# Kernel tuning notes

Hardware: AMD Instinct MI355X
Metric: run time of the kernel (lower is better)

Reference implementation:

```python
import jax, jax.numpy as jnp
import numpy as np

N, E, D, H = 100000, 1250000, 64, 128
EPS = 1e-5


def sage_bn_relu(x, src, dst, W_self, b_self, W_neigh, gamma, beta):
    # mean aggregation over in-neighbors (DGL SAGEConv 'mean')
    n = x.shape[0]
    deg = jax.ops.segment_sum(jnp.ones((src.shape[0],), x.dtype), dst, num_segments=n)
    agg = jax.ops.segment_sum(x[src], dst, num_segments=n)  # [N, d]
    neigh = agg / jnp.maximum(deg, 1.0)[:, None]             # zero in-degree -> 0
    h = x @ W_self + b_self + neigh @ W_neigh                # fc_self + fc_neigh
    # BatchNorm1d (training-mode batch statistics, biased variance)
    mu = h.mean(0)
    var = jnp.mean((h - mu) ** 2, axis=0)
    h = (h - mu) * jax.lax.rsqrt(var + EPS) * gamma + beta
    return jax.nn.relu(h)  # dropout omitted (deterministic eval)


def setup_inputs() -> dict:
    key = jax.random.key(0)
    ks = jax.random.split(key, 32)
    inp = {
        "x": jax.random.normal(ks[0], (N, D), jnp.float32),
        "src": jax.random.randint(ks[1], (E,), 0, N),
        "dst": jax.random.randint(ks[2], (E,), 0, N),
    }
    dims = [(D, H), (H, H), (H, H)]
    k = 3
    for i, (din, dout) in enumerate(dims):
        s = 1.0 / np.sqrt(din)
        inp[f"W_self{i}"] = jax.random.uniform(ks[k], (din, dout), jnp.float32, -s, s); k += 1
        inp[f"b_self{i}"] = jnp.zeros((dout,), jnp.float32)
        inp[f"W_neigh{i}"] = jax.random.uniform(ks[k], (din, dout), jnp.float32, -s, s); k += 1
        inp[f"gamma{i}"] = jnp.ones((dout,), jnp.float32)
        inp[f"beta{i}"] = jnp.zeros((dout,), jnp.float32)
    s = 1.0 / np.sqrt(H)
    inp["Wc"] = jax.random.uniform(ks[k], (H, 2), jnp.float32, -s, s)
    inp["bc"] = jnp.zeros((2,), jnp.float32)
    return inp


def reference(x, src, dst,
              W_self0, b_self0, W_neigh0, gamma0, beta0,
              W_self1, b_self1, W_neigh1, gamma1, beta1,
              W_self2, b_self2, W_neigh2, gamma2, beta2,
              Wc, bc):
    h = sage_bn_relu(x, src, dst, W_self0, b_self0, W_neigh0, gamma0, beta0)
    h = sage_bn_relu(h, src, dst, W_self1, b_self1, W_neigh1, gamma1, beta1)
    h = sage_bn_relu(h, src, dst, W_self2, b_self2, W_neigh2, gamma2, beta2)
    return h @ Wc + bc  # [N, 2]
```

## Files before the change

kernel.cpp:

```cpp
#include <hip/hip_runtime.h>


#define N_NODES 100000
#define N_EDGES 1250000
#define NB 1563
#define BSZ 64
#define CAP 1024
#define BPART 256
#define INVN (1.0f / 100000.0f)

typedef short bf16x8 __attribute__((ext_vector_type(8)));
typedef float f32x4 __attribute__((ext_vector_type(4)));
typedef unsigned short u16x8 __attribute__((ext_vector_type(8)));
typedef unsigned short u16x4 __attribute__((ext_vector_type(4)));

__device__ __forceinline__ float bf2f(unsigned short u) {
  union { unsigned int i; float f; } c; c.i = ((unsigned int)u) << 16; return c.f;
}
__device__ __forceinline__ unsigned short f2bf(float f) {
  union { float f; unsigned int i; } c; c.f = f;
  unsigned int r = (c.i + 0x7FFFu + ((c.i >> 16) & 1u)) >> 16;
  return (unsigned short)r;
}
__device__ __forceinline__ void bn_st(const float* stats, const float* gam,
                                      const float* bet, int c, float& s, float& t) {
  float sum = stats[c] + stats[256 + c] + stats[512 + c] + stats[768 + c];
  float sq  = stats[128 + c] + stats[384 + c] + stats[640 + c] + stats[896 + c];
  float mu = sum * INVN;
  float var = sq * INVN - mu * mu;
  s = gam[c] * rsqrtf(var + 1e-5f);
  t = bet[c] - mu * s;
}
__device__ __forceinline__ void gload_lds16(const void* g, void* l) {
  __builtin_amdgcn_global_load_lds(
      (const __attribute__((address_space(1))) unsigned int*)g,
      (__attribute__((address_space(3))) unsigned int*)l, 16, 0, 0);
}

__global__ __launch_bounds__(256) void k_prep(
    const float* __restrict__ x, unsigned short* __restrict__ x16,
    const float* __restrict__ W0s, const float* __restrict__ W0n,
    const float* __restrict__ W1s, const float* __restrict__ W1n,
    const float* __restrict__ W2s, const float* __restrict__ W2n,
    unsigned short* __restrict__ wt, float* __restrict__ stats3,
    const int* __restrict__ dst, int* __restrict__ hist, int E) {
  __shared__ int hh[NB];
  int blk = blockIdx.x, t = threadIdx.x;
  if (blk < 6250) {
    int i = blk * 256 + t;
    float4 v = ((const float4*)x)[i];
    u16x4 o;
    o.x = f2bf(v.x); o.y = f2bf(v.y); o.z = f2bf(v.z); o.w = f2bf(v.w);
    ((u16x4*)x16)[i] = o;
  } else if (blk < 6570) {
    int i = (blk - 6250) * 256 + t;
    if (i < 16384) {
      const float* W = (i < 8192) ? W0s : W0n;
      unsigned short* o = wt + (i < 8192 ? 0 : 8192);
      int j = i & 8191;
      int c = j >> 6, k = j & 63;
      o[j] = f2bf(W[k * 128 + c]);
    } else {
      int j = i - 16384;
      int sel = j >> 14;
      j &= 16383;
      const float* W = (sel == 0) ? W1s : (sel == 1) ? W1n : (sel == 2) ? W2s : W2n;
      unsigned short* o = wt + 16384 + sel * 16384;
      int c = j >> 7, k = j & 127;
      o[j] = f2bf(W[k * 128 + c]);
    }
  } else if (blk == 6570) {
    for (int i = t; i < 3 * 1024; i += 256) stats3[i] = 0.f;
  } else {
    int hb = blk - 6571;
    int chunk = (E + BPART - 1) / BPART;
    int start = hb * chunk;
    int end = min(E, start + chunk);
    for (int b = t; b < NB; b += 256) hh[b] = 0;
    __syncthreads();
    for (int e = start + t; e < end; e += 256) atomicAdd(&hh[dst[e] >> 6], 1);
    __syncthreads();
    for (int b = t; b < NB; b += 256) hist[hb * NB + b] = hh[b];
  }
}

__global__ __launch_bounds__(256) void k_scan(const int* __restrict__ hist,
                                              int* __restrict__ base,
                                              int* __restrict__ gcursor) {
  int bb = blockIdx.x * 256 + threadIdx.x;
  if (bb >= NB) return;
  int run = 0;
  for (int r0 = 0; r0 < BPART; r0 += 16) {
    int v[16];
    #pragma unroll
    for (int u = 0; u < 16; u++) v[u] = hist[(r0 + u) * NB + bb];
    #pragma unroll
    for (int u = 0; u < 16; u++) { base[(r0 + u) * NB + bb] = run; run += v[u]; }
  }
  gcursor[bb] = run;
}

__global__ __launch_bounds__(256) void k_scatter(const int* __restrict__ src,
                                                 const int* __restrict__ dst,
                                                 const int* __restrict__ base,
                                                 unsigned int* __restrict__ part, int E) {
  __shared__ int cur[NB];
  int t = threadIdx.x;
  int chunk = (E + BPART - 1) / BPART;
  int start = blockIdx.x * chunk;
  int end = min(E, start + chunk);
  for (int b = t; b < NB; b += 256) cur[b] = base[blockIdx.x * NB + b];
  __syncthreads();
  for (int e = start + t; e < end; e += 256) {
    int d = dst[e];
    int b = d >> 6;
    int pos = atomicAdd(&cur[b], 1);
    if ((unsigned)pos < (unsigned)CAP)
      part[(size_t)b * CAP + pos] = (unsigned)src[e] | ((unsigned)(d & 63) << 17);
  }
}

template <int DIN, bool BN>
__global__ __launch_bounds__(512, 8) void k_layer(
    const unsigned short* __restrict__ h, const unsigned short* __restrict__ W1t,
    const unsigned short* __restrict__ W2t, const float* __restrict__ bias,
    const unsigned int* __restrict__ part, const int* __restrict__ gcursor,
    unsigned short* __restrict__ C, float* __restrict__ stats, int M,
    const float* __restrict__ statsP, const float* __restrict__ gamP,
    const float* __restrict__ betP) {
  __shared__ unsigned short neighT[64 * DIN];
  __shared__ unsigned eord[CAP];
  __shared__ unsigned short Bs[2][128 * 32];
  __shared__ int cnt[BSZ], offv[BSZ], cur[BSZ];
  __shared__ int stealCtr;
  __shared__ float sBN[128], tBN[128];
  unsigned* eraw = (unsigned*)neighT;
  float* redS = (float*)eord;
  float* redQ = redS + 512;

  constexpr int SWZM = (DIN == 128) ? 15 : 7;
  constexpr int KS = DIN / 32;
  int t = threadIdx.x;
  int lane = t & 63, w = t >> 6;
  int l15 = lane & 15, quad = lane >> 4;
  int bkt = blockIdx.x;
  int node0 = bkt * BSZ;
  int nn = min(BSZ, M - node0);

  if (t < BSZ) cnt[t] = 0;
  if (t == 0) stealCtr = 0;
  if (BN && t < 128) bn_st(statsP, gamP, betP, t, sBN[t], tBN[t]);
  __syncthreads();

  int ec = gcursor[bkt];
  ec = max(0, min(ec, CAP));
  for (int i = t; i < ec; i += 512) {
    unsigned wd = part[(size_t)bkt * CAP + i];
    eraw[i] = wd;
    atomicAdd(&cnt[wd >> 17], 1);
  }
  __syncthreads();
  if (t < BSZ) offv[t] = cnt[t];
  __syncthreads();
  #pragma unroll
  for (int o = 1; o < BSZ; o <<= 1) {
    int xv = 0;
    if (t < BSZ && t >= o) xv = offv[t - o];
    __syncthreads();
    if (t < BSZ) offv[t] += xv;
    __syncthreads();
  }
  if (t < BSZ) { int ex = offv[t] - cnt[t]; offv[t] = ex; cur[t] = ex; }
  __syncthreads();
  for (int i = t; i < ec; i += 512) {
    unsigned wd = eraw[i];
    int p = atomicAdd(&cur[wd >> 17], 1);
    eord[p] = wd & 0x1FFFF;
  }
  __syncthreads();

  const int strip = w >> 1;
  const int ch = w & 1;
  const int row = strip * 16 + l15;
  f32x4 acc4[4];
  #pragma unroll
  for (int ct = 0; ct < 4; ct++) acc4[ct] = (f32x4){0.f, 0.f, 0.f, 0.f};
  #pragma unroll
  for (int s = 0; s < KS; s++) {
    int k0 = s * 32;
    u16x8 v = *(const u16x8*)&h[(size_t)(node0 + row) * DIN + k0 + quad * 8];
    if (BN) {
      #pragma unroll
      for (int j = 0; j < 8; j++) {
        int c = k0 + quad * 8 + j;
        v[j] = f2bf(fmaxf(fmaf(bf2f(v[j]), sBN[c], tBN[c]), 0.f));
      }
    }
    bf16x8 af = *(bf16x8*)&v;
    #pragma unroll
    for (int ct = 0; ct < 4; ct++) {
      u16x8 bv = *(const u16x8*)&W1t[(size_t)(ch * 64 + ct * 16 + l15) * DIN + k0 + quad * 8];
      acc4[ct] = __builtin_amdgcn_mfma_f32_16x16x32_bf16(af, *(bf16x8*)&bv, acc4[ct], 0, 0, 0);
    }
  }

  const int G = DIN / 8;
  int li = t & (G - 1);
  float sreg[8], treg[8];
  if (BN) {
    #pragma unroll
    for (int k = 0; k < 8; k++) { sreg[k] = sBN[li * 8 + k]; treg[k] = tBN[li * 8 + k]; }
  }
  for (;;) {
    int nd0 = 0;
    if (li == 0) nd0 = atomicAdd(&stealCtr, 1);
    int nd = __shfl(nd0, 0, G);
    if (nd >= BSZ) break;
    u16x8 o;
    if (nd >= nn) {
      #pragma unroll
      for (int k = 0; k < 8; k++) o[k] = 0;
    } else {
      int s = offv[nd], c = cnt[nd];
      int e = s + c;
      float acc[8] = {0.f, 0.f, 0.f, 0.f, 0.f, 0.f, 0.f, 0.f};
      int j = s;
      for (; j + 2 <= e; j += 2) {
        int sn0 = eord[j], sn1 = eord[j + 1];
        u16x8 v0 = *(const u16x8*)&h[(size_t)sn0 * DIN + li * 8];
        u16x8 v1 = *(const u16x8*)&h[(size_t)sn1 * DIN + li * 8];
        if (BN) {
          #pragma unroll
          for (int k = 0; k < 8; k++)
            acc[k] += fmaxf(fmaf(bf2f(v0[k]), sreg[k], treg[k]), 0.f)
                    + fmaxf(fmaf(bf2f(v1[k]), sreg[k], treg[k]), 0.f);
        } else {
          #pragma unroll
          for (int k = 0; k < 8; k++) acc[k] += bf2f(v0[k]) + bf2f(v1[k]);
        }
      }
      if (j < e) {
        int sn = eord[j];
        u16x8 v = *(const u16x8*)&h[(size_t)sn * DIN + li * 8];
        if (BN) {
          #pragma unroll
          for (int k = 0; k < 8; k++)
            acc[k] += fmaxf(fmaf(bf2f(v[k]), sreg[k], treg[k]), 0.f);
        } else {
          #pragma unroll
          for (int k = 0; k < 8; k++) acc[k] += bf2f(v[k]);
        }
      }
      float inv = 1.0f / fmaxf((float)c, 1.0f);
      #pragma unroll
      for (int k = 0; k < 8; k++) o[k] = f2bf(acc[k] * inv);
    }
    *(u16x8*)&neighT[nd * DIN + ((li * 8) ^ ((nd & SWZM) << 3))] = o;
  }

  auto stageBs = [&](int k0, int bi) {
    int r = t >> 2, c = t & 3;
    int p = c ^ ((r >> 1) & 3);
    gload_lds16(&W2t[(size_t)r * DIN + k0 + p * 8], &Bs[bi][(w * 64) * 8]);
  };
  stageBs(0, 0);
  __syncthreads();

  int cb = 0;
  #pragma unroll
  for (int s = 0; s < KS; s++) {
    if (s + 1 < KS) stageBs((s + 1) * 32, cb ^ 1);
    int cc = s * 32 + quad * 8;
    u16x8 v = *(const u16x8*)&neighT[row * DIN + (cc ^ ((row & SWZM) << 3))];
    bf16x8 af = *(bf16x8*)&v;
    #pragma unroll
    for (int ct = 0; ct < 4; ct++) {
      int brow = ch * 64 + ct * 16 + l15;
      bf16x8 bfr = *(const bf16x8*)&Bs[cb][brow * 32 + ((quad ^ ((brow >> 1) & 3)) * 8)];
      acc4[ct] = __builtin_amdgcn_mfma_f32_16x16x32_bf16(af, bfr, acc4[ct], 0, 0, 0);
    }
    if (s + 1 < KS) __syncthreads();
    cb ^= 1;
  }

  float bcol[4], ls[4], lq[4];
  #pragma unroll
  for (int ct = 0; ct < 4; ct++) {
    bcol[ct] = bias[ch * 64 + ct * 16 + l15];
    ls[ct] = 0.f; lq[ct] = 0.f;
  }
  #pragma unroll
  for (int r = 0; r < 4; r++) {
    int orow = node0 + strip * 16 + quad * 4 + r;
    if (orow < M) {
      #pragma unroll
      for (int ct = 0; ct < 4; ct++) {
        float v = acc4[ct][r] + bcol[ct];
        C[(size_t)orow * 128 + ch * 64 + ct * 16 + l15] = f2bf(v);
        ls[ct] += v; lq[ct] += v * v;
      }
    }
  }
  __syncthreads();
  #pragma unroll
  for (int ct = 0; ct < 4; ct++) {
    ls[ct] += __shfl_xor(ls[ct], 16); ls[ct] += __shfl_xor(ls[ct], 32);
    lq[ct] += __shfl_xor(lq[ct], 16); lq[ct] += __shfl_xor(lq[ct], 32);
  }
  if (quad == 0) {
    #pragma unroll
    for (int ct = 0; ct < 4; ct++) {
      redS[w * 64 + ct * 16 + l15] = ls[ct];
      redQ[w * 64 + ct * 16 + l15] = lq[ct];
    }
  }
  __syncthreads();
  if (t < 128) {
    int ch2 = t >> 6, c6 = t & 63;
    float s = 0.f, q = 0.f;
    #pragma unroll
    for (int st = 0; st < 4; st++) {
      s += redS[(st * 2 + ch2) * 64 + c6];
      q += redQ[(st * 2 + ch2) * 64 + c6];
    }
    int rep = (bkt & 3) * 256;
    atomicAdd(&stats[rep + t], s);
    atomicAdd(&stats[rep + 128 + t], q);
  }
}

__global__ void k_final(const unsigned short* __restrict__ h,
                        const float* __restrict__ statsP, const float* __restrict__ gamP,
                        const float* __restrict__ betP, const float* __restrict__ Wc,
                        const float* __restrict__ bc, float* __restrict__ out, int n) {
  int lane = threadIdx.x & 63;
  int row = blockIdx.x * (blockDim.x >> 6) + (threadIdx.x >> 6);
  if (row >= n) return;
  float acc0 = 0.f, acc1 = 0.f;
  #pragma unroll
  for (int m = 0; m < 2; m++) {
    int c = lane + 64 * m;
    float s, tt;
    bn_st(statsP, gamP, betP, c, s, tt);
    float v = bf2f(h[(size_t)row * 128 + c]);
    v = fmaxf(fmaf(v, s, tt), 0.f);
    acc0 += v * Wc[c * 2 + 0];
    acc1 += v * Wc[c * 2 + 1];
  }
  #pragma unroll
  for (int off = 32; off > 0; off >>= 1) {
    acc0 += __shfl_down(acc0, off);
    acc1 += __shfl_down(acc1, off);
  }
  if (lane == 0) {
    out[row * 2 + 0] = acc0 + bc[0];
    out[row * 2 + 1] = acc1 + bc[1];
  }
}

extern "C" void kernel_launch(void* const* d_in, const int* in_sizes, int n_in,
                              void* d_out, int out_size, void* d_ws, size_t ws_size,
                              hipStream_t stream) {
  const float* x   = (const float*)d_in[0];
  const int* src   = (const int*)d_in[1];
  const int* dst   = (const int*)d_in[2];
  const float* Wself[3] = {(const float*)d_in[3], (const float*)d_in[8],  (const float*)d_in[13]};
  const float* bself[3] = {(const float*)d_in[4], (const float*)d_in[9],  (const float*)d_in[14]};
  const float* Wngh[3]  = {(const float*)d_in[5], (const float*)d_in[10], (const float*)d_in[15]};
  const float* gam[3]   = {(const float*)d_in[6], (const float*)d_in[11], (const float*)d_in[16]};
  const float* bet[3]   = {(const float*)d_in[7], (const float*)d_in[12], (const float*)d_in[17]};
  const float* Wc = (const float*)d_in[18];
  const float* bc = (const float*)d_in[19];
  float* out = (float*)d_out;

  const int N = N_NODES, E = N_EDGES;

  unsigned short* x16 = (unsigned short*)d_ws;
  unsigned short* b0  = x16 + (size_t)N * 64;
  unsigned short* b1  = b0 + (size_t)N * 128;
  unsigned short* b2  = b1 + (size_t)N * 128;
  unsigned short* wt  = b2 + (size_t)N * 128;
  unsigned int* part  = (unsigned int*)(wt + 81920);
  int* gcursor  = (int*)(part + (size_t)NB * CAP);
  float* stats3 = (float*)(gcursor + NB);

  int* hist = (int*)b1;
  int* base = hist + (size_t)BPART * NB;

  k_prep<<<6571 + BPART, 256, 0, stream>>>(
      x, x16, Wself[0], Wngh[0], Wself[1], Wngh[1], Wself[2], Wngh[2],
      wt, stats3, dst, hist, E);

  k_scan<<<(NB + 255) / 256, 256, 0, stream>>>(hist, base, gcursor);
  k_scatter<<<BPART, 256, 0, stream>>>(src, dst, base, part, E);

  k_layer<64, false><<<NB, 512, 0, stream>>>(
      x16, wt + 0, wt + 8192, bself[0], part, gcursor, b1, stats3 + 0, N,
      nullptr, nullptr, nullptr);
  k_layer<128, true><<<NB, 512, 0, stream>>>(
      b1, wt + 16384, wt + 32768, bself[1], part, gcursor, b2, stats3 + 1024, N,
      stats3 + 0, gam[0], bet[0]);
  k_layer<128, true><<<NB, 512, 0, stream>>>(
      b2, wt + 49152, wt + 65536, bself[2], part, gcursor, b1, stats3 + 2048, N,
      stats3 + 1024, gam[1], bet[1]);

  k_final<<<(N + 3) / 4, 256, 0, stream>>>(b1, stats3 + 2048, gam[2], bet[2],
                                           Wc, bc, out, N);
}
```

Measured before the change: 410.0 us.

## Stage both weight matrices through double-buffered LDS and use wave-shuffle prefix scan

Replaces the multi-barrier LDS Hillis-Steele scan over bucket counts with a single-wave shuffle-up scan. The self-term GEMM, which loaded W1t straight from global memory before aggregation, now runs after aggregation in one 2*KS-step double-buffered loop that stages W1t and then W2t into LDS. The XOR swizzle on the B tile is dropped, which may bring LDS bank conflicts back, and one barrier before the stats reduction is removed. Keeping the self-term accumulators out of the aggregation loop may also lower register pressure.

```diff
diff --git a/kernel.cpp b/kernel.cpp
--- a/kernel.cpp
+++ b/kernel.cpp
@@ -160,17 +160,17 @@
     atomicAdd(&cnt[wd >> 17], 1);
   }
   __syncthreads();
-  if (t < BSZ) offv[t] = cnt[t];
-  __syncthreads();
-  #pragma unroll
-  for (int o = 1; o < BSZ; o <<= 1) {
-    int xv = 0;
-    if (t < BSZ && t >= o) xv = offv[t - o];
-    __syncthreads();
-    if (t < BSZ) offv[t] += xv;
-    __syncthreads();
-  }
-  if (t < BSZ) { int ex = offv[t] - cnt[t]; offv[t] = ex; cur[t] = ex; }
+  if (w == 0) {
+    int v = cnt[lane];
+    int incl = v;
+    #pragma unroll
+    for (int o = 1; o < 64; o <<= 1) {
+      int u = __shfl_up(incl, o);
+      if (lane >= o) incl += u;
+    }
+    offv[lane] = incl - v;
+    cur[lane] = incl - v;
+  }
   __syncthreads();
   for (int i = t; i < ec; i += 512) {
     unsigned wd = eraw[i];
@@ -178,31 +178,6 @@
     eord[p] = wd & 0x1FFFF;
   }
   __syncthreads();
-
-  const int strip = w >> 1;
-  const int ch = w & 1;
-  const int row = strip * 16 + l15;
-  f32x4 acc4[4];
-  #pragma unroll
-  for (int ct = 0; ct < 4; ct++) acc4[ct] = (f32x4){0.f, 0.f, 0.f, 0.f};
-  #pragma unroll
-  for (int s = 0; s < KS; s++) {
-    int k0 = s * 32;
-    u16x8 v = *(const u16x8*)&h[(size_t)(node0 + row) * DIN + k0 + quad * 8];
-    if (BN) {
-      #pragma unroll
-      for (int j = 0; j < 8; j++) {
-        int c = k0 + quad * 8 + j;
-        v[j] = f2bf(fmaxf(fmaf(bf2f(v[j]), sBN[c], tBN[c]), 0.f));
-      }
-    }
-    bf16x8 af = *(bf16x8*)&v;
-    #pragma unroll
-    for (int ct = 0; ct < 4; ct++) {
-      u16x8 bv = *(const u16x8*)&W1t[(size_t)(ch * 64 + ct * 16 + l15) * DIN + k0 + quad * 8];
-      acc4[ct] = __builtin_amdgcn_mfma_f32_16x16x32_bf16(af, *(bf16x8*)&bv, acc4[ct], 0, 0, 0);
-    }
-  }
 
   const int G = DIN / 8;
   int li = t & (G - 1);
@@ -258,28 +233,49 @@
     *(u16x8*)&neighT[nd * DIN + ((li * 8) ^ ((nd & SWZM) << 3))] = o;
   }
 
-  auto stageBs = [&](int k0, int bi) {
-    int r = t >> 2, c = t & 3;
-    int p = c ^ ((r >> 1) & 3);
-    gload_lds16(&W2t[(size_t)r * DIN + k0 + p * 8], &Bs[bi][(w * 64) * 8]);
+  const int strip = w >> 1;
+  const int ch = w & 1;
+  const int row = strip * 16 + l15;
+  f32x4 acc4[4];
+  #pragma unroll
+  for (int ct = 0; ct < 4; ct++) acc4[ct] = (f32x4){0.f, 0.f, 0.f, 0.f};
+
+  auto stageBs = [&](int s, int bi) {
+    const unsigned short* Wt = (s < KS) ? W1t : W2t;
+    int k0 = ((s < KS) ? s : s - KS) * 32;
+    int r = t >> 2, prt = t & 3;
+    gload_lds16(&Wt[(size_t)r * DIN + k0 + prt * 8], &Bs[bi][(w * 64) * 8]);
   };
   stageBs(0, 0);
   __syncthreads();
 
   int cb = 0;
   #pragma unroll
-  for (int s = 0; s < KS; s++) {
-    if (s + 1 < KS) stageBs((s + 1) * 32, cb ^ 1);
-    int cc = s * 32 + quad * 8;
-    u16x8 v = *(const u16x8*)&neighT[row * DIN + (cc ^ ((row & SWZM) << 3))];
-    bf16x8 af = *(bf16x8*)&v;
+  for (int s = 0; s < 2 * KS; s++) {
+    if (s + 1 < 2 * KS) stageBs(s + 1, cb ^ 1);
+    bf16x8 af;
+    if (s < KS) {
+      int k0 = s * 32;
+      u16x8 v = *(const u16x8*)&h[(size_t)(node0 + row) * DIN + k0 + quad * 8];
+      if (BN) {
+        #pragma unroll
+        for (int j = 0; j < 8; j++) {
+          int c = k0 + quad * 8 + j;
+          v[j] = f2bf(fmaxf(fmaf(bf2f(v[j]), sBN[c], tBN[c]), 0.f));
+        }
+      }
+      af = *(bf16x8*)&v;
+    } else {
+      int cc = (s - KS) * 32 + quad * 8;
+      u16x8 v = *(const u16x8*)&neighT[row * DIN + (cc ^ ((row & SWZM) << 3))];
+      af = *(bf16x8*)&v;
+    }
     #pragma unroll
     for (int ct = 0; ct < 4; ct++) {
-      int brow = ch * 64 + ct * 16 + l15;
-      bf16x8 bfr = *(const bf16x8*)&Bs[cb][brow * 32 + ((quad ^ ((brow >> 1) & 3)) * 8)];
+      bf16x8 bfr = *(const bf16x8*)&Bs[cb][(ch * 64 + ct * 16 + l15) * 32 + quad * 8];
       acc4[ct] = __builtin_amdgcn_mfma_f32_16x16x32_bf16(af, bfr, acc4[ct], 0, 0, 0);
     }
-    if (s + 1 < KS) __syncthreads();
+    if (s + 1 < 2 * KS) __syncthreads();
     cb ^= 1;
   }
 
@@ -301,7 +297,6 @@
       }
     }
   }
-  __syncthreads();
   #pragma unroll
   for (int ct = 0; ct < 4; ct++) {
     ls[ct] += __shfl_xor(ls[ct], 16); ls[ct] += __shfl_xor(ls[ct], 32);
```

Result: faster. 368.8 us (-10.0%).
